# Kernel optimization log

Measured on AMD Instinct MI355X. Metric: run time of the kernel, lower is better.

The kernel has to match this reference:

```python
import jax, jax.numpy as jnp
import numpy as np

B, C, H, W = 16, 64, 128, 128
E = 8          # number of experts
TOPK = 2       # num_expert (top-k routing)


def setup_inputs() -> dict:
    key = jax.random.key(0)
    ks = jax.random.split(key, 8)
    s = 1.0 / np.sqrt(C)
    x = jax.random.normal(ks[0], (B, C, H, W), dtype=jnp.float32)
    k = jax.random.normal(ks[1], (B, C, 1, 1), dtype=jnp.float32)
    Wg = jax.random.normal(ks[2], (C, E), dtype=jnp.float32) * s
    bg = jnp.zeros((E,), dtype=jnp.float32)
    W1 = jax.random.normal(ks[3], (E, C, C), dtype=jnp.float32) * s  # [E, out, in]
    b1 = jnp.zeros((E, C), dtype=jnp.float32)
    W2 = jax.random.normal(ks[4], (E, C, C), dtype=jnp.float32) * s
    b2 = jnp.zeros((E, C), dtype=jnp.float32)
    return {"x": x, "k": k, "Wg": Wg, "bg": bg, "W1": W1, "b1": b1, "W2": W2, "b2": b2}


def reference(x, k, Wg, bg, W1, b1, W2, b2):
    # --- gate: global avg pool + linear -> [B, E] logits ---
    pooled = x.mean(axis=(2, 3))                              # [B, C]
    logits = pooled @ Wg + bg                                  # [B, E]
    # softmax in fp32 then cast back (matches F.softmax(dtype=torch.float).to(x.dtype))
    weights = jax.nn.softmax(logits.astype(jnp.float32), axis=1).astype(x.dtype)
    topk_w, topk_idx = jax.lax.top_k(weights, TOPK)           # [B, TOPK]
    # scatter top-k weights into dense per-expert mask [B, E]
    mask = jnp.zeros_like(weights).at[jnp.arange(B)[:, None], topk_idx].set(topk_w)
    # --- training branch: run ALL experts, combine with mask ---
    # expert_e(x, k) = W2_e @ gelu((W1_e @ x + b1_e) * k) + b2_e   (1x1 convs)
    h = jnp.einsum('eoc,bchw->ebohw', W1, x) + b1[:, None, :, None, None]
    h = jax.nn.gelu(h * k[None])                               # [E, B, C, H, W]
    y = jnp.einsum('eoc,ebchw->ebohw', W2, h) + b2[:, None, :, None, None]
    out = x + jnp.einsum('ebchw,be->bchw', y, mask)
    return out
```

## Files before the change

### kernel.cpp

```cpp
#include <hip/hip_runtime.h>
#include <hip/hip_bf16.h>


#define BB 16
#define CC 64
#define EE 8
#define HWPX 16384
#define NT 4

typedef __bf16 bf16x8 __attribute__((ext_vector_type(8)));
typedef float f32x4 __attribute__((ext_vector_type(4)));

__device__ __forceinline__ unsigned packbf2(float lo, float hi) {
    __bf16 a = (__bf16)lo, b = (__bf16)hi;
    unsigned short ua = __builtin_bit_cast(unsigned short, a);
    unsigned short ub = __builtin_bit_cast(unsigned short, b);
    return ((unsigned)ub << 16) | (unsigned)ua;
}

__device__ __forceinline__ int swz(int px, int d) {
    return px * 32 + ((d & ~3) ^ ((px & 7) << 2)) + (d & 3);
}

__global__ __launch_bounds__(256) void pool_conv_kernel(
    const float* __restrict__ x, float* __restrict__ pooled,
    const float* __restrict__ W1, const float* __restrict__ W2,
    __bf16* __restrict__ W1b, __bf16* __restrict__ W2b) {
    int blk = blockIdx.x;
    if (blk < BB * CC) {
        const float4* p = (const float4*)(x + (size_t)blk * HWPX);
        float s = 0.f;
        for (int i = threadIdx.x; i < HWPX / 4; i += 256) {
            float4 v = p[i];
            s += (v.x + v.y) + (v.z + v.w);
        }
        #pragma unroll
        for (int off = 32; off > 0; off >>= 1) s += __shfl_down(s, off);
        __shared__ float ls[4];
        if ((threadIdx.x & 63) == 0) ls[threadIdx.x >> 6] = s;
        __syncthreads();
        if (threadIdx.x == 0) pooled[blk] = ((ls[0] + ls[1]) + (ls[2] + ls[3])) * (1.0f / (float)HWPX);
    } else {
        int i = (blk - BB * CC) * 256 + threadIdx.x;
        W1b[i] = (__bf16)W1[i];
        W2b[i] = (__bf16)W2[i];
    }
}

__global__ void gate_kernel(const float* __restrict__ pooled,
                            const float* __restrict__ Wg,
                            const float* __restrict__ bg,
                            int* __restrict__ gidx, float* __restrict__ gw) {
    int b = threadIdx.x;
    if (b >= BB) return;
    float logits[EE];
    #pragma unroll
    for (int e = 0; e < EE; ++e) logits[e] = bg[e];
    for (int c = 0; c < CC; ++c) {
        float pv = pooled[b * CC + c];
        #pragma unroll
        for (int e = 0; e < EE; ++e) logits[e] = fmaf(pv, Wg[c * EE + e], logits[e]);
    }
    float m = logits[0];
    #pragma unroll
    for (int e = 1; e < EE; ++e) m = fmaxf(m, logits[e]);
    float w[EE]; float den = 0.f;
    #pragma unroll
    for (int e = 0; e < EE; ++e) { w[e] = expf(logits[e] - m); den += w[e]; }
    float inv = 1.0f / den;
    #pragma unroll
    for (int e = 0; e < EE; ++e) w[e] *= inv;
    int i0 = 0;
    #pragma unroll
    for (int e = 1; e < EE; ++e) if (w[e] > w[i0]) i0 = e;
    int i1 = -1;
    #pragma unroll
    for (int e = 0; e < EE; ++e) {
        if (e == i0) continue;
        if (i1 < 0 || w[e] > w[i1]) i1 = e;
    }
    gidx[b * 2 + 0] = i0; gidx[b * 2 + 1] = i1;
    gw[b * 2 + 0] = w[i0]; gw[b * 2 + 1] = w[i1];
}

__global__ __launch_bounds__(256) void moe_main(
    const float* __restrict__ x, const float* __restrict__ kvec,
    const __bf16* __restrict__ W1b, const float* __restrict__ b1,
    const __bf16* __restrict__ W2b, const float* __restrict__ b2,
    const int* __restrict__ gidx, const float* __restrict__ gw,
    float* __restrict__ out) {

    __shared__ unsigned int LA[64 * 32];
    __shared__ unsigned int LB[64 * 32];

    const int blk = blockIdx.x;
    const int b = blk >> 6;
    const int P0 = (blk & 63) << 8;
    const int t = threadIdx.x;
    const int w = t >> 6;
    const int l = t & 63;
    const int g = l >> 4;
    const int l15 = l & 15;

    const int arow = 16 * w + l15;
    const int r0w = 16 * w + 4 * g;
    const int d0 = 8 * w + 2 * g;

    const int e0 = __builtin_amdgcn_readfirstlane(gidx[b * 2 + 0]);
    const int e1 = __builtin_amdgcn_readfirstlane(gidx[b * 2 + 1]);
    const float wgt0 = gw[b * 2 + 0];
    const float wgt1 = gw[b * 2 + 1];

    const float* xb = x + b * CC * HWPX;
    float* ob = out + b * CC * HWPX;
    const int obase = r0w * HWPX + P0 + l15;

    float xc[16];
    #pragma unroll
    for (int cb = 0; cb < 4; ++cb)
        #pragma unroll
        for (int j = 0; j < 4; ++j)
            xc[cb * 4 + j] = xb[obase + j * HWPX + cb * 16];

    bf16x8 a1f[2][2], a2f[2][2];
    #pragma unroll
    for (int ks = 0; ks < 2; ++ks) {
        a1f[0][ks] = *(const bf16x8*)(W1b + e0 * CC * CC + arow * CC + ks * 32 + g * 8);
        a1f[1][ks] = *(const bf16x8*)(W1b + e1 * CC * CC + arow * CC + ks * 32 + g * 8);
        a2f[0][ks] = *(const bf16x8*)(W2b + e0 * CC * CC + arow * CC + ks * 32 + g * 8);
        a2f[1][ks] = *(const bf16x8*)(W2b + e1 * CC * CC + arow * CC + ks * 32 + g * 8);
    }
    const f32x4 b1v0 = *(const f32x4*)(b1 + e0 * CC + r0w);
    const f32x4 b1v1 = *(const f32x4*)(b1 + e1 * CC + r0w);
    const f32x4 b2v0 = *(const f32x4*)(b2 + e0 * CC + r0w);
    const f32x4 b2v1 = *(const f32x4*)(b2 + e1 * CC + r0w);
    const f32x4 kk   = *(const f32x4*)(kvec + b * CC + r0w);

    float bsum[4];
    #pragma unroll
    for (int j = 0; j < 4; ++j) bsum[j] = fmaf(wgt0, b2v0[j], wgt1 * b2v1[j]);

    const float C1 = -2.302208239f;
    const float C2 = -0.1029434f;

    #pragma unroll
    for (int cb = 0; cb < 4; ++cb) {
        uint2 pk;
        pk.x = packbf2(xc[cb * 4 + 0], xc[cb * 4 + 1]);
        pk.y = packbf2(xc[cb * 4 + 2], xc[cb * 4 + 3]);
        *(uint2*)&LA[swz(cb * 16 + l15, d0)] = pk;
    }
    __syncthreads();

    #pragma unroll
    for (int it = 0; it < NT; ++it) {
        unsigned int* XT = (it & 1) ? LB : LA;
        unsigned int* H0 = (it & 1) ? LA : LB;

        float xn[16];
        if (it < NT - 1) {
            #pragma unroll
            for (int cb = 0; cb < 4; ++cb)
                #pragma unroll
                for (int j = 0; j < 4; ++j)
                    xn[cb * 4 + j] = xb[obase + (it + 1) * 64 + j * HWPX + cb * 16];
        }

        bf16x8 bx[4][2];
        #pragma unroll
        for (int cb = 0; cb < 4; ++cb)
            #pragma unroll
            for (int ks = 0; ks < 2; ++ks)
                bx[cb][ks] = *(const bf16x8*)&XT[swz(cb * 16 + l15, ks * 16 + g * 4)];

        f32x4 h0[4], h1[4];
        #pragma unroll
        for (int cb = 0; cb < 4; ++cb) {
            h0[cb] = (f32x4){0.f, 0.f, 0.f, 0.f};
            h1[cb] = (f32x4){0.f, 0.f, 0.f, 0.f};
            #pragma unroll
            for (int ks = 0; ks < 2; ++ks) {
                h0[cb] = __builtin_amdgcn_mfma_f32_16x16x32_bf16(a1f[0][ks], bx[cb][ks], h0[cb], 0, 0, 0);
                h1[cb] = __builtin_amdgcn_mfma_f32_16x16x32_bf16(a1f[1][ks], bx[cb][ks], h1[cb], 0, 0, 0);
            }
        }

        uint2 p0k[4], p1k[4];
        #pragma unroll
        for (int cb = 0; cb < 4; ++cb) {
            float hv0[4], hv1[4];
            #pragma unroll
            for (int j = 0; j < 4; ++j) {
                float t0 = (h0[cb][j] + b1v0[j]) * kk[j];
                float ex0 = __builtin_amdgcn_exp2f(t0 * fmaf(C2, t0 * t0, C1));
                hv0[j] = (t0 * wgt0) * __builtin_amdgcn_rcpf(ex0 + 1.f);
                float t1 = (h1[cb][j] + b1v1[j]) * kk[j];
                float ex1 = __builtin_amdgcn_exp2f(t1 * fmaf(C2, t1 * t1, C1));
                hv1[j] = (t1 * wgt1) * __builtin_amdgcn_rcpf(ex1 + 1.f);
            }
            p0k[cb].x = packbf2(hv0[0], hv0[1]);
            p0k[cb].y = packbf2(hv0[2], hv0[3]);
            p1k[cb].x = packbf2(hv1[0], hv1[1]);
            p1k[cb].y = packbf2(hv1[2], hv1[3]);
        }

        #pragma unroll
        for (int cb = 0; cb < 4; ++cb)
            *(uint2*)&H0[swz(cb * 16 + l15, d0)] = p0k[cb];
        __syncthreads();

        #pragma unroll
        for (int cb = 0; cb < 4; ++cb)
            *(uint2*)&XT[swz(cb * 16 + l15, d0)] = p1k[cb];

        f32x4 acc[4];
        #pragma unroll
        for (int cb = 0; cb < 4; ++cb) {
            acc[cb] = (f32x4){0.f, 0.f, 0.f, 0.f};
            #pragma unroll
            for (int ks = 0; ks < 2; ++ks) {
                bf16x8 bh = *(const bf16x8*)&H0[swz(cb * 16 + l15, ks * 16 + g * 4)];
                acc[cb] = __builtin_amdgcn_mfma_f32_16x16x32_bf16(a2f[0][ks], bh, acc[cb], 0, 0, 0);
            }
        }
        __syncthreads();

        if (it < NT - 1) {
            #pragma unroll
            for (int cb = 0; cb < 4; ++cb) {
                uint2 pk;
                pk.x = packbf2(xn[cb * 4 + 0], xn[cb * 4 + 1]);
                pk.y = packbf2(xn[cb * 4 + 2], xn[cb * 4 + 3]);
                *(uint2*)&H0[swz(cb * 16 + l15, d0)] = pk;
            }
        }

        #pragma unroll
        for (int cb = 0; cb < 4; ++cb) {
            #pragma unroll
            for (int ks = 0; ks < 2; ++ks) {
                bf16x8 bh = *(const bf16x8*)&XT[swz(cb * 16 + l15, ks * 16 + g * 4)];
                acc[cb] = __builtin_amdgcn_mfma_f32_16x16x32_bf16(a2f[1][ks], bh, acc[cb], 0, 0, 0);
            }
        }

        #pragma unroll
        for (int cb = 0; cb < 4; ++cb)
            #pragma unroll
            for (int j = 0; j < 4; ++j)
                ob[obase + it * 64 + j * HWPX + cb * 16] = xc[cb * 4 + j] + (acc[cb][j] + bsum[j]);

        if (it < NT - 1) {
            #pragma unroll
            for (int i = 0; i < 16; ++i) xc[i] = xn[i];
            __syncthreads();
        }
    }
}

extern "C" void kernel_launch(void* const* d_in, const int* in_sizes, int n_in,
                              void* d_out, int out_size, void* d_ws, size_t ws_size,
                              hipStream_t stream) {
    const float* x  = (const float*)d_in[0];
    const float* k  = (const float*)d_in[1];
    const float* Wg = (const float*)d_in[2];
    const float* bg = (const float*)d_in[3];
    const float* W1 = (const float*)d_in[4];
    const float* b1 = (const float*)d_in[5];
    const float* W2 = (const float*)d_in[6];
    const float* b2 = (const float*)d_in[7];
    float* out = (float*)d_out;

    float*  pooled = (float*)d_ws;
    int*    gidx   = (int*)((char*)d_ws + 4096);
    float*  gw     = (float*)((char*)d_ws + 4096 + 128);
    __bf16* W1b    = (__bf16*)((char*)d_ws + 8192);
    __bf16* W2b    = (__bf16*)((char*)d_ws + 8192 + 65536);

    pool_conv_kernel<<<BB * CC + EE * CC * CC / 256, 256, 0, stream>>>(x, pooled, W1, W2, W1b, W2b);
    gate_kernel<<<1, 64, 0, stream>>>(pooled, Wg, bg, gidx, gw);
    moe_main<<<BB * 64, 256, 0, stream>>>(x, k, W1b, b1, W2b, b2, gidx, gw, out);
}
```

Measured before the change: 51.15 us.

## Split MoE main kernel into one 64-pixel tile per block, dropping the loop

Each moe_main block previously looped over four 64-pixel tiles with register prefetch and ping-pong shared buffers. Now each block handles a single 64-pixel tile, with separate LDS buffers for x and both expert hidden activations, and the grid is four times larger. This gives more blocks for latency hiding and removes the extra barriers and buffer reuse. In exchange, every block reloads the expert weight fragments and biases, and the software prefetch overlap is lost.

```diff
diff --git a/kernel.cpp b/kernel.cpp
--- a/kernel.cpp
+++ b/kernel.cpp
@@ -6,7 +6,6 @@
 #define CC 64
 #define EE 8
 #define HWPX 16384
-#define NT 4
 
 typedef __bf16 bf16x8 __attribute__((ext_vector_type(8)));
 typedef float f32x4 __attribute__((ext_vector_type(4)));
@@ -90,12 +89,13 @@
     const int* __restrict__ gidx, const float* __restrict__ gw,
     float* __restrict__ out) {
 
-    __shared__ unsigned int LA[64 * 32];
-    __shared__ unsigned int LB[64 * 32];
+    __shared__ unsigned int LX[64 * 32];
+    __shared__ unsigned int LH0[64 * 32];
+    __shared__ unsigned int LH1[64 * 32];
 
     const int blk = blockIdx.x;
-    const int b = blk >> 6;
-    const int P0 = (blk & 63) << 8;
+    const int b = blk >> 8;
+    const int P0 = (blk & 255) << 6;
     const int t = threadIdx.x;
     const int w = t >> 6;
     const int l = t & 63;
@@ -111,17 +111,6 @@
     const float wgt0 = gw[b * 2 + 0];
     const float wgt1 = gw[b * 2 + 1];
 
-    const float* xb = x + b * CC * HWPX;
-    float* ob = out + b * CC * HWPX;
-    const int obase = r0w * HWPX + P0 + l15;
-
-    float xc[16];
-    #pragma unroll
-    for (int cb = 0; cb < 4; ++cb)
-        #pragma unroll
-        for (int j = 0; j < 4; ++j)
-            xc[cb * 4 + j] = xb[obase + j * HWPX + cb * 16];
-
     bf16x8 a1f[2][2], a2f[2][2];
     #pragma unroll
     for (int ks = 0; ks < 2; ++ks) {
@@ -135,127 +124,85 @@
     const f32x4 b2v0 = *(const f32x4*)(b2 + e0 * CC + r0w);
     const f32x4 b2v1 = *(const f32x4*)(b2 + e1 * CC + r0w);
     const f32x4 kk   = *(const f32x4*)(kvec + b * CC + r0w);
-
     float bsum[4];
     #pragma unroll
     for (int j = 0; j < 4; ++j) bsum[j] = fmaf(wgt0, b2v0[j], wgt1 * b2v1[j]);
 
-    const float C1 = -2.302208239f;
-    const float C2 = -0.1029434f;
+    const float* xb = x + b * CC * HWPX;
+    const int obase = r0w * HWPX + P0 + l15;
+    float xc[16];
+    #pragma unroll
+    for (int cb = 0; cb < 4; ++cb)
+        #pragma unroll
+        for (int j = 0; j < 4; ++j)
+            xc[cb * 4 + j] = xb[obase + j * HWPX + cb * 16];
 
     #pragma unroll
     for (int cb = 0; cb < 4; ++cb) {
         uint2 pk;
         pk.x = packbf2(xc[cb * 4 + 0], xc[cb * 4 + 1]);
         pk.y = packbf2(xc[cb * 4 + 2], xc[cb * 4 + 3]);
-        *(uint2*)&LA[swz(cb * 16 + l15, d0)] = pk;
+        *(uint2*)&LX[swz(cb * 16 + l15, d0)] = pk;
     }
     __syncthreads();
 
-    #pragma unroll
-    for (int it = 0; it < NT; ++it) {
-        unsigned int* XT = (it & 1) ? LB : LA;
-        unsigned int* H0 = (it & 1) ? LA : LB;
-
-        float xn[16];
-        if (it < NT - 1) {
-            #pragma unroll
-            for (int cb = 0; cb < 4; ++cb)
-                #pragma unroll
-                for (int j = 0; j < 4; ++j)
-                    xn[cb * 4 + j] = xb[obase + (it + 1) * 64 + j * HWPX + cb * 16];
+    f32x4 h0[4], h1[4];
+    #pragma unroll
+    for (int cb = 0; cb < 4; ++cb) {
+        bf16x8 bx0 = *(const bf16x8*)&LX[swz(cb * 16 + l15, g * 4)];
+        bf16x8 bx1 = *(const bf16x8*)&LX[swz(cb * 16 + l15, 16 + g * 4)];
+        h0[cb] = (f32x4){0.f, 0.f, 0.f, 0.f};
+        h1[cb] = (f32x4){0.f, 0.f, 0.f, 0.f};
+        h0[cb] = __builtin_amdgcn_mfma_f32_16x16x32_bf16(a1f[0][0], bx0, h0[cb], 0, 0, 0);
+        h0[cb] = __builtin_amdgcn_mfma_f32_16x16x32_bf16(a1f[0][1], bx1, h0[cb], 0, 0, 0);
+        h1[cb] = __builtin_amdgcn_mfma_f32_16x16x32_bf16(a1f[1][0], bx0, h1[cb], 0, 0, 0);
+        h1[cb] = __builtin_amdgcn_mfma_f32_16x16x32_bf16(a1f[1][1], bx1, h1[cb], 0, 0, 0);
+    }
+
+    const float C1 = -2.302208239f;
+    const float C2 = -0.1029434f;
+
+    #pragma unroll
+    for (int cb = 0; cb < 4; ++cb) {
+        float hv0[4], hv1[4];
+        #pragma unroll
+        for (int j = 0; j < 4; ++j) {
+            float t0 = (h0[cb][j] + b1v0[j]) * kk[j];
+            float ex0 = __builtin_amdgcn_exp2f(t0 * fmaf(C2, t0 * t0, C1));
+            hv0[j] = (t0 * wgt0) * __builtin_amdgcn_rcpf(ex0 + 1.f);
+            float t1 = (h1[cb][j] + b1v1[j]) * kk[j];
+            float ex1 = __builtin_amdgcn_exp2f(t1 * fmaf(C2, t1 * t1, C1));
+            hv1[j] = (t1 * wgt1) * __builtin_amdgcn_rcpf(ex1 + 1.f);
         }
-
-        bf16x8 bx[4][2];
-        #pragma unroll
-        for (int cb = 0; cb < 4; ++cb)
-            #pragma unroll
-            for (int ks = 0; ks < 2; ++ks)
-                bx[cb][ks] = *(const bf16x8*)&XT[swz(cb * 16 + l15, ks * 16 + g * 4)];
-
-        f32x4 h0[4], h1[4];
-        #pragma unroll
-        for (int cb = 0; cb < 4; ++cb) {
-            h0[cb] = (f32x4){0.f, 0.f, 0.f, 0.f};
-            h1[cb] = (f32x4){0.f, 0.f, 0.f, 0.f};
-            #pragma unroll
-            for (int ks = 0; ks < 2; ++ks) {
-                h0[cb] = __builtin_amdgcn_mfma_f32_16x16x32_bf16(a1f[0][ks], bx[cb][ks], h0[cb], 0, 0, 0);
-                h1[cb] = __builtin_amdgcn_mfma_f32_16x16x32_bf16(a1f[1][ks], bx[cb][ks], h1[cb], 0, 0, 0);
-            }
+        uint2 pk0, pk1;
+        pk0.x = packbf2(hv0[0], hv0[1]);
+        pk0.y = packbf2(hv0[2], hv0[3]);
+        pk1.x = packbf2(hv1[0], hv1[1]);
+        pk1.y = packbf2(hv1[2], hv1[3]);
+        *(uint2*)&LH0[swz(cb * 16 + l15, d0)] = pk0;
+        *(uint2*)&LH1[swz(cb * 16 + l15, d0)] = pk1;
+    }
+    __syncthreads();
+
+    f32x4 acc[4];
+    #pragma unroll
+    for (int cb = 0; cb < 4; ++cb) {
+        acc[cb] = (f32x4){0.f, 0.f, 0.f, 0.f};
+        #pragma unroll
+        for (int ks = 0; ks < 2; ++ks) {
+            bf16x8 bh0 = *(const bf16x8*)&LH0[swz(cb * 16 + l15, ks * 16 + g * 4)];
+            acc[cb] = __builtin_amdgcn_mfma_f32_16x16x32_bf16(a2f[0][ks], bh0, acc[cb], 0, 0, 0);
+            bf16x8 bh1 = *(const bf16x8*)&LH1[swz(cb * 16 + l15, ks * 16 + g * 4)];
+            acc[cb] = __builtin_amdgcn_mfma_f32_16x16x32_bf16(a2f[1][ks], bh1, acc[cb], 0, 0, 0);
         }
-
-        uint2 p0k[4], p1k[4];
-        #pragma unroll
-        for (int cb = 0; cb < 4; ++cb) {
-            float hv0[4], hv1[4];
-            #pragma unroll
-            for (int j = 0; j < 4; ++j) {
-                float t0 = (h0[cb][j] + b1v0[j]) * kk[j];
-                float ex0 = __builtin_amdgcn_exp2f(t0 * fmaf(C2, t0 * t0, C1));
-                hv0[j] = (t0 * wgt0) * __builtin_amdgcn_rcpf(ex0 + 1.f);
-                float t1 = (h1[cb][j] + b1v1[j]) * kk[j];
-                float ex1 = __builtin_amdgcn_exp2f(t1 * fmaf(C2, t1 * t1, C1));
-                hv1[j] = (t1 * wgt1) * __builtin_amdgcn_rcpf(ex1 + 1.f);
-            }
-            p0k[cb].x = packbf2(hv0[0], hv0[1]);
-            p0k[cb].y = packbf2(hv0[2], hv0[3]);
-            p1k[cb].x = packbf2(hv1[0], hv1[1]);
-            p1k[cb].y = packbf2(hv1[2], hv1[3]);
-        }
-
-        #pragma unroll
-        for (int cb = 0; cb < 4; ++cb)
-            *(uint2*)&H0[swz(cb * 16 + l15, d0)] = p0k[cb];
-        __syncthreads();
-
-        #pragma unroll
-        for (int cb = 0; cb < 4; ++cb)
-            *(uint2*)&XT[swz(cb * 16 + l15, d0)] = p1k[cb];
-
-        f32x4 acc[4];
-        #pragma unroll
-        for (int cb = 0; cb < 4; ++cb) {
-            acc[cb] = (f32x4){0.f, 0.f, 0.f, 0.f};
-            #pragma unroll
-            for (int ks = 0; ks < 2; ++ks) {
-                bf16x8 bh = *(const bf16x8*)&H0[swz(cb * 16 + l15, ks * 16 + g * 4)];
-                acc[cb] = __builtin_amdgcn_mfma_f32_16x16x32_bf16(a2f[0][ks], bh, acc[cb], 0, 0, 0);
-            }
-        }
-        __syncthreads();
-
-        if (it < NT - 1) {
-            #pragma unroll
-            for (int cb = 0; cb < 4; ++cb) {
-                uint2 pk;
-                pk.x = packbf2(xn[cb * 4 + 0], xn[cb * 4 + 1]);
-                pk.y = packbf2(xn[cb * 4 + 2], xn[cb * 4 + 3]);
-                *(uint2*)&H0[swz(cb * 16 + l15, d0)] = pk;
-            }
-        }
-
-        #pragma unroll
-        for (int cb = 0; cb < 4; ++cb) {
-            #pragma unroll
-            for (int ks = 0; ks < 2; ++ks) {
-                bf16x8 bh = *(const bf16x8*)&XT[swz(cb * 16 + l15, ks * 16 + g * 4)];
-                acc[cb] = __builtin_amdgcn_mfma_f32_16x16x32_bf16(a2f[1][ks], bh, acc[cb], 0, 0, 0);
-            }
-        }
-
-        #pragma unroll
-        for (int cb = 0; cb < 4; ++cb)
-            #pragma unroll
-            for (int j = 0; j < 4; ++j)
-                ob[obase + it * 64 + j * HWPX + cb * 16] = xc[cb * 4 + j] + (acc[cb][j] + bsum[j]);
-
-        if (it < NT - 1) {
-            #pragma unroll
-            for (int i = 0; i < 16; ++i) xc[i] = xn[i];
-            __syncthreads();
-        }
-    }
+    }
+
+    float* ob = out + b * CC * HWPX;
+    #pragma unroll
+    for (int cb = 0; cb < 4; ++cb)
+        #pragma unroll
+        for (int j = 0; j < 4; ++j)
+            ob[obase + j * HWPX + cb * 16] = xc[cb * 4 + j] + (acc[cb][j] + bsum[j]);
 }
 
 extern "C" void kernel_launch(void* const* d_in, const int* in_sizes, int n_in,
@@ -279,5 +226,5 @@
 
     pool_conv_kernel<<<BB * CC + EE * CC * CC / 256, 256, 0, stream>>>(x, pooled, W1, W2, W1b, W2b);
     gate_kernel<<<1, 64, 0, stream>>>(pooled, Wg, bg, gidx, gw);
-    moe_main<<<BB * 64, 256, 0, stream>>>(x, k, W1b, b1, W2b, b2, gidx, gw, out);
-}
+    moe_main<<<BB * 256, 256, 0, stream>>>(x, k, W1b, b1, W2b, b2, gidx, gw, out);
+}
```

Result: no change. 51.55 us (+0.8%).
